# Kernel optimization log

Measured on AMD Instinct MI355X. Metric: run time of the kernel, lower is better.

Reference implementation:

```python
import jax, jax.numpy as jnp
import numpy as np

DIM = 768
NUM_HEADS = 16
HEAD_DIM = DIM // NUM_HEADS  # 48


def setup_inputs() -> dict:
    key = jax.random.key(0)
    ks = jax.random.split(key, 9)
    s = 1.0 / np.sqrt(DIM)
    return {
        "x": jax.random.normal(ks[0], (4, 2048, DIM), dtype=jnp.float32),
        "Wq": jax.random.uniform(ks[1], (DIM, DIM), jnp.float32, -s, s),
        "bq": jax.random.uniform(ks[2], (DIM,), jnp.float32, -s, s),
        "Wk": jax.random.uniform(ks[3], (DIM, DIM), jnp.float32, -s, s),
        "bk": jax.random.uniform(ks[4], (DIM,), jnp.float32, -s, s),
        "Wv": jax.random.uniform(ks[5], (DIM, DIM), jnp.float32, -s, s),
        "bv": jax.random.uniform(ks[6], (DIM,), jnp.float32, -s, s),
        "Wo": jax.random.uniform(ks[7], (DIM, DIM), jnp.float32, -s, s),
        "bo": jax.random.uniform(ks[8], (DIM,), jnp.float32, -s, s),
    }


def reference(x, Wq, bq, Wk, bk, Wv, bv, Wo, bo):
    B, S, D = x.shape
    H, Dh = NUM_HEADS, HEAD_DIM
    # qkv projections -> [B, H, S, Dh]
    q = (x @ Wq.T + bq).reshape(B, S, H, Dh).transpose(0, 2, 1, 3)
    k = (x @ Wk.T + bk).reshape(B, S, H, Dh).transpose(0, 2, 1, 3)
    v = (x @ Wv.T + bv).reshape(B, S, H, Dh).transpose(0, 2, 1, 3)
    scale = 1.0 / np.sqrt(Dh).astype(np.float32)
    scores = jnp.einsum('bhqd,bhkd->bhqk', q, k) * scale  # [B,H,S,S]
    attn = jax.nn.softmax(scores, axis=-1)
    # dropout is identity in eval mode
    out = jnp.einsum('bhqk,bhkd->bhqd', attn, v)  # [B,H,S,Dh]
    out = out.transpose(0, 2, 1, 3).reshape(B, S, D)
    return out @ Wo.T + bo
```

## Files before the change

### kernel.cpp

```cpp
#include <hip/hip_runtime.h>
#include <cstdint>
#include <cstddef>


typedef short s8v __attribute__((ext_vector_type(8)));
typedef float f4v __attribute__((ext_vector_type(4)));
typedef float f16v __attribute__((ext_vector_type(16)));

static constexpr int Bn = 4, Sn = 2048, Dn = 768, Hn = 16, DhN = 48, Dp = 64;
static constexpr int MS = Bn * Sn;

#define MFMA16(a, b, c) __builtin_amdgcn_mfma_f32_16x16x32_bf16((a), (b), (c), 0, 0, 0)
#define MFMA32(a, b, c) __builtin_amdgcn_mfma_f32_32x32x16_bf16((a), (b), (c), 0, 0, 0)

__device__ __forceinline__ int swz4(int r) { return (r + (r >> 2)) & 3; }

__device__ __forceinline__ ushort f2b(float f) {
  return (ushort)((__builtin_bit_cast(uint32_t, f) + 0x8000u) >> 16);
}
__device__ __forceinline__ uint32_t packbf(float a, float b) {
  uint32_t ua = __builtin_bit_cast(uint32_t, a) + 0x8000u;
  uint32_t ub = __builtin_bit_cast(uint32_t, b) + 0x8000u;
  return __builtin_amdgcn_perm(ub, ua, 0x07060302u);
}
__device__ __forceinline__ void pl32swap(uint32_t& a, uint32_t& b) {
  asm("v_permlane32_swap_b32 %0, %1" : "+v"(a), "+v"(b));
}
__device__ __forceinline__ float fexp2(float x) {
  return __builtin_amdgcn_exp2f(x);
}
__device__ __forceinline__ void gload_lds16(const ushort* g, ushort* l) {
  __builtin_amdgcn_global_load_lds(
      (const __attribute__((address_space(1))) uint32_t*)g,
      (__attribute__((address_space(3))) uint32_t*)l, 16, 0, 0);
}

__global__ void cvt_all(const float* __restrict__ x,
                        const float* __restrict__ wq, const float* __restrict__ wk,
                        const float* __restrict__ wv, const float* __restrict__ wo,
                        ushort* __restrict__ xb, ushort* __restrict__ wqkv,
                        ushort* __restrict__ wob) {
  const int bid = blockIdx.x;
  const float* src;
  ushort* dst;
  int i;
  if (bid < 6144) {
    src = x; dst = xb; i = bid * 256 + threadIdx.x;
  } else {
    const int r = (bid - 6144) / 576;
    i = ((bid - 6144) % 576) * 256 + threadIdx.x;
    src = (r == 0) ? wq : (r == 1) ? wk : (r == 2) ? wv : wo;
    dst = (r < 3) ? (wqkv + (size_t)r * Dn * Dn) : wob;
  }
  float4 f = ((const float4*)src)[i];
  ushort4 o = { f2b(f.x), f2b(f.y), f2b(f.z), f2b(f.w) };
  ((ushort4*)dst)[i] = o;
}

__global__ __launch_bounds__(256) void gemm_qkv(
    const ushort* __restrict__ A, const ushort* __restrict__ W,
    const float* __restrict__ bq, const float* __restrict__ bk, const float* __restrict__ bv,
    ushort* __restrict__ outq, ushort* __restrict__ outk, ushort* __restrict__ outv,
    float qscale) {
  __shared__ __align__(16) ushort As[128][64];
  __shared__ __align__(16) ushort Bs[128][64];
  const int tid = threadIdx.x, lane = tid & 63, wave = tid >> 6;
  const int l15 = lane & 15, g = lane >> 4;
  const int m0 = blockIdx.y * 128, n0 = blockIdx.x * 128;
  const int wqm = (wave >> 1) * 64;
  const int wqx = (wave & 1) * 64;
  f4v acc[4][4] = {};

  const ushort* agp[4];
  const ushort* bgp[4];
  ushort* lap[4];
  ushort* lbp[4];
#pragma unroll
  for (int q = 0; q < 4; ++q) {
    const int slot = q * 256 + wave * 64 + lane;
    const int r = slot >> 3, sc = slot & 7;
    const int u = ((((sc & 3) ^ swz4(r & 15)) | (sc & 4)) ^ ((r & 1) << 2)) * 8;
    agp[q] = A + (size_t)(m0 + r) * Dn + u;
    bgp[q] = W + (size_t)(n0 + r) * Dn + u;
    lap[q] = &As[0][0] + slot * 8;
    lbp[q] = &Bs[0][0] + slot * 8;
  }
  const int fcol = (g ^ swz4(l15)) * 8;
  const int par = l15 & 1;

  for (int k0 = 0; k0 < Dn; k0 += 64) {
    __syncthreads();
#pragma unroll
    for (int q = 0; q < 4; ++q) {
      gload_lds16(agp[q] + k0, lap[q]);
      gload_lds16(bgp[q] + k0, lbp[q]);
    }
    __syncthreads();
#pragma unroll
    for (int h = 0; h < 2; ++h) {
      const int fc = fcol + 32 * (h ^ par);
      s8v wf[4], xf[4];
#pragma unroll
      for (int i = 0; i < 4; ++i) wf[i] = *(const s8v*)&Bs[wqm + i * 16 + l15][fc];
#pragma unroll
      for (int j = 0; j < 4; ++j) xf[j] = *(const s8v*)&As[wqx + j * 16 + l15][fc];
#pragma unroll
      for (int i = 0; i < 4; ++i)
#pragma unroll
        for (int j = 0; j < 4; ++j) acc[i][j] = MFMA16(wf[i], xf[j], acc[i][j]);
    }
  }

  const int region = blockIdx.x / 6;
  const int nbase = n0 - region * 768;
  const float* bias = (region == 0) ? bq : (region == 1) ? bk : bv;
#pragma unroll
  for (int i = 0; i < 4; ++i) {
    const int n = nbase + wqm + i * 16 + g * 4;
    const float4 b4 = *(const float4*)&bias[n];
    const int h = n / DhN, dh = n - h * DhN;
#pragma unroll
    for (int j = 0; j < 4; ++j) {
      const int s = m0 + wqx + j * 16 + l15;
      const int b = s >> 11, srow = s & 2047;
      const int bh = b * Hn + h;
      float v0 = acc[i][j][0] + b4.x, v1 = acc[i][j][1] + b4.y;
      float v2 = acc[i][j][2] + b4.z, v3 = acc[i][j][3] + b4.w;
      if (region == 0) { v0 *= qscale; v1 *= qscale; v2 *= qscale; v3 *= qscale; }
      if (region < 2) {
        ushort4 o = { f2b(v0), f2b(v1), f2b(v2), f2b(v3) };
        ushort* dst = region ? outk : outq;
        *(ushort4*)&dst[((size_t)bh * Sn + srow) * Dp + dh] = o;
      } else {
        outv[((size_t)bh * DhN + dh + 0) * Sn + srow] = f2b(v0);
        outv[((size_t)bh * DhN + dh + 1) * Sn + srow] = f2b(v1);
        outv[((size_t)bh * DhN + dh + 2) * Sn + srow] = f2b(v2);
        outv[((size_t)bh * DhN + dh + 3) * Sn + srow] = f2b(v3);
      }
    }
  }
}

__global__ __launch_bounds__(256) void gemm_out(
    const ushort* __restrict__ A, const ushort* __restrict__ W,
    const float* __restrict__ bias, float* __restrict__ out) {
  __shared__ __align__(16) ushort As[128][64];
  __shared__ __align__(16) ushort Bs[128][64];
  const int tid = threadIdx.x, lane = tid & 63, wave = tid >> 6;
  const int l15 = lane & 15, g = lane >> 4;
  const int m0 = blockIdx.y * 128, n0 = blockIdx.x * 128;
  const int wqm = (wave >> 1) * 64;
  const int wqx = (wave & 1) * 64;
  f4v acc[4][4] = {};

  const ushort* agp[4];
  const ushort* bgp[4];
  ushort* lap[4];
  ushort* lbp[4];
#pragma unroll
  for (int q = 0; q < 4; ++q) {
    const int slot = q * 256 + wave * 64 + lane;
    const int r = slot >> 3, sc = slot & 7;
    const int u = ((((sc & 3) ^ swz4(r & 15)) | (sc & 4)) ^ ((r & 1) << 2)) * 8;
    agp[q] = A + (size_t)(m0 + r) * Dn + u;
    bgp[q] = W + (size_t)(n0 + r) * Dn + u;
    lap[q] = &As[0][0] + slot * 8;
    lbp[q] = &Bs[0][0] + slot * 8;
  }
  const int fcol = (g ^ swz4(l15)) * 8;
  const int par = l15 & 1;

  for (int k0 = 0; k0 < Dn; k0 += 64) {
    __syncthreads();
#pragma unroll
    for (int q = 0; q < 4; ++q) {
      gload_lds16(agp[q] + k0, lap[q]);
      gload_lds16(bgp[q] + k0, lbp[q]);
    }
    __syncthreads();
#pragma unroll
    for (int h = 0; h < 2; ++h) {
      const int fc = fcol + 32 * (h ^ par);
      s8v wf[4], xf[4];
#pragma unroll
      for (int i = 0; i < 4; ++i) wf[i] = *(const s8v*)&Bs[wqm + i * 16 + l15][fc];
#pragma unroll
      for (int j = 0; j < 4; ++j) xf[j] = *(const s8v*)&As[wqx + j * 16 + l15][fc];
#pragma unroll
      for (int i = 0; i < 4; ++i)
#pragma unroll
        for (int j = 0; j < 4; ++j) acc[i][j] = MFMA16(wf[i], xf[j], acc[i][j]);
    }
  }

#pragma unroll
  for (int i = 0; i < 4; ++i) {
    const int n = n0 + wqm + i * 16 + g * 4;
    const float4 b4 = *(const float4*)&bias[n];
#pragma unroll
    for (int j = 0; j < 4; ++j) {
      const int s = m0 + wqx + j * 16 + l15;
      float4 o4 = { acc[i][j][0] + b4.x, acc[i][j][1] + b4.y,
                    acc[i][j][2] + b4.z, acc[i][j][3] + b4.w };
      *(float4*)&out[(size_t)s * Dn + n] = o4;
    }
  }
}

__global__ __launch_bounds__(256) void attn_kernel(
    const ushort* __restrict__ qg, const ushort* __restrict__ kg,
    const ushort* __restrict__ vg, ushort* __restrict__ og) {
  __shared__ __align__(16) ushort Ka[128][32];
  __shared__ __align__(16) ushort Kb[128][16];
  __shared__ __align__(16) ushort Vs[64][128];
  const int tid = threadIdx.x;
  const int lane = tid & 63;
  const int wave = tid >> 6;
  const int l31 = lane & 31;
  const int h = lane >> 5;
  const int lin = blockIdx.x + (blockIdx.y << 4);
  const int k8 = lin >> 3;
  const int bh = (lin & 7) * 8 + (k8 >> 4);
  const int q0 = (k8 & 15) * 128;
  const ushort* qb = qg + (size_t)bh * Sn * Dp;
  const ushort* kb = kg + (size_t)bh * Sn * Dp;
  const ushort* vb = vg + (size_t)bh * DhN * Sn;

#pragma unroll
  for (int t = 0; t < 4; ++t) {
    const int idx = tid + t * 256;
    const int row = 48 + (idx >> 6);
    ((uint32_t*)&Vs[row][0])[idx & 63] = (row == 48) ? 0x3F803F80u : 0u;
  }

  s8v qf[3];
#pragma unroll
  for (int kc = 0; kc < 3; ++kc)
    qf[kc] = *(const s8v*)(qb + (size_t)(q0 + wave * 32 + l31) * Dp + kc * 16 + h * 8);

  const ushort* gsrc[6];
  ushort* ldst[6];
  int gstep[6];
#pragma unroll
  for (int t = 0; t < 6; ++t) {
    const int c = wave + 4 * t;
    if (c < 8) {
      const int row = 16 * c + (lane >> 2), j = lane & 3;
      gsrc[t] = kb + (size_t)row * Dp + (j ^ ((row >> 1) & 3)) * 8;
      ldst[t] = &Ka[0][0] + 16 * c * 32 + lane * 8;
      gstep[t] = 128 * Dp;
    } else if (c < 12) {
      const int row = 32 * (c - 8) + (lane >> 1), j = lane & 1;
      gsrc[t] = kb + (size_t)row * Dp + 32 + (j ^ ((row >> 2) & 1)) * 8;
      ldst[t] = &Kb[0][0] + 32 * (c - 8) * 16 + lane * 8;
      gstep[t] = 128 * Dp;
    } else {
      const int row = 4 * (c - 12) + (lane >> 4), j = lane & 15;
      gsrc[t] = vb + (size_t)row * Sn + (j ^ (row & 7)) * 8;
      ldst[t] = &Vs[0][0] + 4 * (c - 12) * 128 + lane * 8;
      gstep[t] = 128;
    }
  }

  f16v o0 = {}, o1 = {};

  for (int kt = 0; kt < Sn; kt += 128) {
    __syncthreads();
#pragma unroll
    for (int t = 0; t < 6; ++t) {
      gload_lds16(gsrc[t], ldst[t]);
      gsrc[t] += gstep[t];
    }
    __syncthreads();

#pragma unroll
    for (int mg = 0; mg < 4; ++mg) {
      const int row = 32 * mg + l31;
      const int s1 = (l31 >> 1) & 3, s2 = (l31 >> 2) & 1;
      s8v a0 = *(const s8v*)&Ka[row][((0 | h) ^ s1) * 8];
      s8v a1 = *(const s8v*)&Ka[row][((2 | h) ^ s1) * 8];
      s8v a2 = *(const s8v*)&Kb[row][((h) ^ s2) * 8];
      f16v sc = {};
      sc = MFMA32(a0, qf[0], sc);
      sc = MFMA32(a1, qf[1], sc);
      sc = MFMA32(a2, qf[2], sc);
      float p[16];
#pragma unroll
      for (int r = 0; r < 16; ++r) p[r] = fexp2(sc[r]);

#pragma unroll
      for (int c2 = 0; c2 < 2; ++c2) {
        const int rb = 8 * c2;
        uint32_t w0 = packbf(p[rb + 0], p[rb + 1]);
        uint32_t w1 = packbf(p[rb + 2], p[rb + 3]);
        uint32_t w2 = packbf(p[rb + 4], p[rb + 5]);
        uint32_t w3 = packbf(p[rb + 6], p[rb + 7]);
        pl32swap(w0, w2);
        pl32swap(w1, w3);
        uint4 af = { w0, w1, w2, w3 };
        const s8v pa = __builtin_bit_cast(s8v, af);
        const int kcv = 2 * mg + c2;
        const int vc = ((2 * kcv + h) ^ (l31 & 7)) * 8;
        const s8v v0 = *(const s8v*)&Vs[l31][vc];
        const s8v v1 = *(const s8v*)&Vs[32 + l31][vc];
        o0 = MFMA32(pa, v0, o0);
        o1 = MFMA32(pa, v1, o1);
      }
    }
  }

  const int b = bh >> 4, hh = bh & 15;
#pragma unroll
  for (int r = 0; r < 16; ++r) {
    const int q = (r & 3) + 8 * (r >> 2) + 4 * h;
    const float lsum = __shfl(o1[r], 16 + (lane & 32), 64);
    const float inv = 1.0f / lsum;
    const int s = q0 + wave * 32 + q;
    const size_t base = ((size_t)(b * Sn + s)) * Dn + hh * DhN;
    og[base + l31] = f2b(o0[r] * inv);
    if (l31 < 16) og[base + 32 + l31] = f2b(o1[r] * inv);
  }
}

extern "C" void kernel_launch(void* const* d_in, const int* in_sizes, int n_in,
                              void* d_out, int out_size, void* d_ws, size_t ws_size,
                              hipStream_t stream) {
  (void)in_sizes; (void)n_in; (void)out_size; (void)ws_size;
  const float* x  = (const float*)d_in[0];
  const float* Wq = (const float*)d_in[1];
  const float* bq = (const float*)d_in[2];
  const float* Wk = (const float*)d_in[3];
  const float* bk = (const float*)d_in[4];
  const float* Wv = (const float*)d_in[5];
  const float* bv = (const float*)d_in[6];
  const float* Wo = (const float*)d_in[7];
  const float* bo = (const float*)d_in[8];

  size_t off = 0;
  auto alloc = [&](size_t bytes) {
    void* p = (char*)d_ws + off;
    off += (bytes + 255) & ~(size_t)255;
    return p;
  };
  ushort* xb    = (ushort*)alloc((size_t)MS * Dn * 2);
  ushort* Wqkvb = (ushort*)alloc((size_t)3 * Dn * Dn * 2);
  ushort* Wob   = (ushort*)alloc((size_t)Dn * Dn * 2);
  ushort* qbuf  = (ushort*)alloc((size_t)Bn * Hn * Sn * Dp * 2);
  ushort* kbuf  = (ushort*)alloc((size_t)Bn * Hn * Sn * Dp * 2);
  ushort* vbuf  = (ushort*)alloc((size_t)Bn * Hn * DhN * Sn * 2);
  ushort* ao    = (ushort*)alloc((size_t)MS * Dn * 2);

  cvt_all<<<6144 + 4 * 576, 256, 0, stream>>>(x, Wq, Wk, Wv, Wo, xb, Wqkvb, Wob);

  const dim3 blk(256);
  const float qscale = 0.20823510929813633f;
  gemm_qkv<<<dim3(18, MS / 128), blk, 0, stream>>>(xb, Wqkvb, bq, bk, bv,
                                                   qbuf, kbuf, vbuf, qscale);

  attn_kernel<<<dim3(Sn / 128, Bn * Hn), blk, 0, stream>>>(qbuf, kbuf, vbuf, ao);

  gemm_out<<<dim3(6, MS / 128), blk, 0, stream>>>(ao, Wob, bo, (float*)d_out);
}
```

Measured before the change: 245.0 us.

## Split attention over key halves with a separate combine kernel

Adds a split-K attention path. Each of two grid slices processes half of the keys and writes unnormalized fp32 partial outputs, with the row sum carried in an extra ones-row of V, to a workspace buffer. A combine kernel then adds the two halves, normalizes and writes bf16. This doubles the number of attention blocks to improve occupancy and load balance across CUs, at the cost of extra global traffic for the partials and one more launch. It relies on there being no running max, so the exp values must stay in range. The path runs only when the workspace is large enough, otherwise it falls back to the original kernel.

```diff
diff --git a/kernel.cpp b/kernel.cpp
--- a/kernel.cpp
+++ b/kernel.cpp
@@ -204,6 +204,142 @@
                     acc[i][j][2] + b4.z, acc[i][j][3] + b4.w };
       *(float4*)&out[(size_t)s * Dn + n] = o4;
     }
+  }
+}
+
+__global__ __launch_bounds__(256) void attn_split(
+    const ushort* __restrict__ qg, const ushort* __restrict__ kg,
+    const ushort* __restrict__ vg, float* __restrict__ pbuf) {
+  __shared__ __align__(16) ushort Ka[64][32];
+  __shared__ __align__(16) ushort Kb[64][16];
+  __shared__ __align__(16) ushort Vs[64][64];
+  const int tid = threadIdx.x;
+  const int lane = tid & 63;
+  const int wave = tid >> 6;
+  const int l31 = lane & 31;
+  const int h = lane >> 5;
+  const int kh = blockIdx.z;
+  const int lin = blockIdx.x + (blockIdx.y << 4);
+  const int k8 = lin >> 3;
+  const int bh = (lin & 7) * 8 + (k8 >> 4);
+  const int q0 = (k8 & 15) * 128;
+  const ushort* qb = qg + (size_t)bh * Sn * Dp;
+  const ushort* kb = kg + (size_t)bh * Sn * Dp + (size_t)kh * 1024 * Dp;
+  const ushort* vb = vg + (size_t)bh * DhN * Sn + kh * 1024;
+
+#pragma unroll
+  for (int t = 0; t < 2; ++t) {
+    const int idx = tid + t * 256;
+    const int row = 48 + (idx >> 5);
+    ((uint32_t*)&Vs[row][0])[idx & 31] = (row == 48) ? 0x3F803F80u : 0u;
+  }
+
+  s8v qf[3];
+#pragma unroll
+  for (int kc = 0; kc < 3; ++kc)
+    qf[kc] = *(const s8v*)(qb + (size_t)(q0 + wave * 32 + l31) * Dp + kc * 16 + h * 8);
+
+  const ushort* gsrc[3];
+  ushort* ldst[3];
+  int gstep[3];
+#pragma unroll
+  for (int t = 0; t < 3; ++t) {
+    const int c = wave + 4 * t;
+    if (c < 4) {
+      const int row = 16 * c + (lane >> 2), j = lane & 3;
+      gsrc[t] = kb + (size_t)row * Dp + (j ^ ((row >> 1) & 3)) * 8;
+      ldst[t] = &Ka[0][0] + 16 * c * 32 + lane * 8;
+      gstep[t] = 64 * Dp;
+    } else if (c < 6) {
+      const int row = 32 * (c - 4) + (lane >> 1), j = lane & 1;
+      gsrc[t] = kb + (size_t)row * Dp + 32 + (j ^ ((row >> 2) & 1)) * 8;
+      ldst[t] = &Kb[0][0] + 32 * (c - 4) * 16 + lane * 8;
+      gstep[t] = 64 * Dp;
+    } else {
+      const int row = 8 * (c - 6) + (lane >> 3), j = lane & 7;
+      gsrc[t] = vb + (size_t)row * Sn + (j ^ (row & 7)) * 8;
+      ldst[t] = &Vs[0][0] + 8 * (c - 6) * 64 + lane * 8;
+      gstep[t] = 64;
+    }
+  }
+
+  f16v o0 = {}, o1 = {};
+
+  for (int kt = 0; kt < 1024; kt += 64) {
+    __syncthreads();
+#pragma unroll
+    for (int t = 0; t < 3; ++t) {
+      gload_lds16(gsrc[t], ldst[t]);
+      gsrc[t] += gstep[t];
+    }
+    __syncthreads();
+
+#pragma unroll
+    for (int mg = 0; mg < 2; ++mg) {
+      const int row = 32 * mg + l31;
+      const int s1 = (l31 >> 1) & 3, s2 = (l31 >> 2) & 1;
+      s8v a0 = *(const s8v*)&Ka[row][((0 | h) ^ s1) * 8];
+      s8v a1 = *(const s8v*)&Ka[row][((2 | h) ^ s1) * 8];
+      s8v a2 = *(const s8v*)&Kb[row][((h) ^ s2) * 8];
+      f16v sc = {};
+      sc = MFMA32(a0, qf[0], sc);
+      sc = MFMA32(a1, qf[1], sc);
+      sc = MFMA32(a2, qf[2], sc);
+      float p[16];
+#pragma unroll
+      for (int r = 0; r < 16; ++r) p[r] = fexp2(sc[r]);
+
+#pragma unroll
+      for (int c2 = 0; c2 < 2; ++c2) {
+        const int rb = 8 * c2;
+        uint32_t w0 = packbf(p[rb + 0], p[rb + 1]);
+        uint32_t w1 = packbf(p[rb + 2], p[rb + 3]);
+        uint32_t w2 = packbf(p[rb + 4], p[rb + 5]);
+        uint32_t w3 = packbf(p[rb + 6], p[rb + 7]);
+        pl32swap(w0, w2);
+        pl32swap(w1, w3);
+        uint4 af = { w0, w1, w2, w3 };
+        const s8v pa = __builtin_bit_cast(s8v, af);
+        const int kcv = 2 * mg + c2;
+        const int vc = ((2 * kcv + h) ^ (l31 & 7)) * 8;
+        const s8v v0 = *(const s8v*)&Vs[l31][vc];
+        const s8v v1 = *(const s8v*)&Vs[32 + l31][vc];
+        o0 = MFMA32(pa, v0, o0);
+        o1 = MFMA32(pa, v1, o1);
+      }
+    }
+  }
+
+  const int qt = q0 >> 7;
+  float* pb = pbuf + ((size_t)kh * 1024 + bh * 16 + qt) * 8192;
+#pragma unroll
+  for (int r = 0; r < 16; ++r) {
+    const int q = (r & 3) + 8 * (r >> 2) + 4 * h;
+    const int sl = wave * 32 + q;
+    pb[sl * 64 + l31] = o0[r];
+    pb[sl * 64 + 32 + l31] = o1[r];
+  }
+}
+
+__global__ __launch_bounds__(256) void attn_combine(
+    const float* __restrict__ pb, ushort* __restrict__ og) {
+  const int bid = blockIdx.x;
+  const int bh = bid >> 4, qt = bid & 15;
+  const int b = bh >> 4, hh = bh & 15;
+  const float* p0 = pb + (size_t)bid * 8192;
+  const float* p1 = p0 + (size_t)1024 * 8192;
+  const int tid = threadIdx.x;
+#pragma unroll
+  for (int it = 0; it < 6; ++it) {
+    const int i4 = tid + 256 * it;
+    const int q = i4 / 12, c4 = i4 - q * 12;
+    const float l = p0[q * 64 + 48] + p1[q * 64 + 48];
+    const float inv = 1.0f / l;
+    const float4 a = *(const float4*)&p0[q * 64 + c4 * 4];
+    const float4 c = *(const float4*)&p1[q * 64 + c4 * 4];
+    ushort4 o = { f2b((a.x + c.x) * inv), f2b((a.y + c.y) * inv),
+                  f2b((a.z + c.z) * inv), f2b((a.w + c.w) * inv) };
+    *(ushort4*)&og[((size_t)(b * Sn + qt * 128 + q)) * Dn + hh * DhN + c4 * 4] = o;
   }
 }
 
@@ -325,7 +461,7 @@
 extern "C" void kernel_launch(void* const* d_in, const int* in_sizes, int n_in,
                               void* d_out, int out_size, void* d_ws, size_t ws_size,
                               hipStream_t stream) {
-  (void)in_sizes; (void)n_in; (void)out_size; (void)ws_size;
+  (void)in_sizes; (void)n_in; (void)out_size;
   const float* x  = (const float*)d_in[0];
   const float* Wq = (const float*)d_in[1];
   const float* bq = (const float*)d_in[2];
@@ -349,6 +485,8 @@
   ushort* kbuf  = (ushort*)alloc((size_t)Bn * Hn * Sn * Dp * 2);
   ushort* vbuf  = (ushort*)alloc((size_t)Bn * Hn * DhN * Sn * 2);
   ushort* ao    = (ushort*)alloc((size_t)MS * Dn * 2);
+  float*  pbuf  = (float*)alloc((size_t)2 * 1024 * 128 * 64 * 4);
+  const bool split = (off <= ws_size);
 
   cvt_all<<<6144 + 4 * 576, 256, 0, stream>>>(x, Wq, Wk, Wv, Wo, xb, Wqkvb, Wob);
 
@@ -357,7 +495,12 @@
   gemm_qkv<<<dim3(18, MS / 128), blk, 0, stream>>>(xb, Wqkvb, bq, bk, bv,
                                                    qbuf, kbuf, vbuf, qscale);
 
-  attn_kernel<<<dim3(Sn / 128, Bn * Hn), blk, 0, stream>>>(qbuf, kbuf, vbuf, ao);
+  if (split) {
+    attn_split<<<dim3(Sn / 128, Bn * Hn, 2), blk, 0, stream>>>(qbuf, kbuf, vbuf, pbuf);
+    attn_combine<<<dim3(Bn * Hn * 16), blk, 0, stream>>>(pbuf, ao);
+  } else {
+    attn_kernel<<<dim3(Sn / 128, Bn * Hn), blk, 0, stream>>>(qbuf, kbuf, vbuf, ao);
+  }
 
   gemm_out<<<dim3(6, MS / 128), blk, 0, stream>>>(ao, Wob, bo, (float*)d_out);
 }
```

New measurement: 255.6 us. 1.04x slower.

## Split attention KV range across two wave groups per block and reduce via LDS

Applied to the files above, without the earlier changes.

The attention kernel now launches 512 threads per block. Two groups of four waves each process half of the key/value sequence, with smaller 64-key tiles staged in separate LDS halves. The partial unnormalized outputs and row sums are combined through LDS scratch before normalization and store. This doubles the waves available per query tile to hide latency, at the cost of extra barriers, an LDS reduction, and more synchronization per iteration.

```diff
diff --git a/kernel.cpp b/kernel.cpp
--- a/kernel.cpp
+++ b/kernel.cpp
@@ -207,15 +207,15 @@
   }
 }
 
-__global__ __launch_bounds__(256) void attn_kernel(
-    const ushort* __restrict__ qg, const ushort* __restrict__ kg,
+__global__ __launch_bounds__(512) void attn_fused(
+    const ushort* __restrict__ qg, const ushort* __restrict__ kgl,
     const ushort* __restrict__ vg, ushort* __restrict__ og) {
-  __shared__ __align__(16) ushort Ka[128][32];
-  __shared__ __align__(16) ushort Kb[128][16];
-  __shared__ __align__(16) ushort Vs[64][128];
+  __shared__ __align__(16) ushort smem[2][7168];
   const int tid = threadIdx.x;
   const int lane = tid & 63;
   const int wave = tid >> 6;
+  const int w4 = wave & 3;
+  const int kg = wave >> 2;
   const int l31 = lane & 31;
   const int h = lane >> 5;
   const int lin = blockIdx.x + (blockIdx.y << 4);
@@ -223,63 +223,62 @@
   const int bh = (lin & 7) * 8 + (k8 >> 4);
   const int q0 = (k8 & 15) * 128;
   const ushort* qb = qg + (size_t)bh * Sn * Dp;
-  const ushort* kb = kg + (size_t)bh * Sn * Dp;
-  const ushort* vb = vg + (size_t)bh * DhN * Sn;
-
-#pragma unroll
-  for (int t = 0; t < 4; ++t) {
-    const int idx = tid + t * 256;
-    const int row = 48 + (idx >> 6);
-    ((uint32_t*)&Vs[row][0])[idx & 63] = (row == 48) ? 0x3F803F80u : 0u;
-  }
+  const ushort* kb = kgl + (size_t)bh * Sn * Dp + (size_t)kg * 1024 * Dp;
+  const ushort* vb = vg + (size_t)bh * DhN * Sn + kg * 1024;
+  ushort* KaH = &smem[kg][0];
+  ushort* KbH = &smem[kg][2048];
+  ushort* VsH = &smem[kg][3072];
+
+  ((uint32_t*)&smem[0][6144])[tid] = (tid < 32) ? 0x3F803F80u : 0u;
+  ((uint32_t*)&smem[1][6144])[tid] = (tid < 32) ? 0x3F803F80u : 0u;
 
   s8v qf[3];
 #pragma unroll
   for (int kc = 0; kc < 3; ++kc)
-    qf[kc] = *(const s8v*)(qb + (size_t)(q0 + wave * 32 + l31) * Dp + kc * 16 + h * 8);
-
-  const ushort* gsrc[6];
-  ushort* ldst[6];
-  int gstep[6];
-#pragma unroll
-  for (int t = 0; t < 6; ++t) {
-    const int c = wave + 4 * t;
-    if (c < 8) {
+    qf[kc] = *(const s8v*)(qb + (size_t)(q0 + w4 * 32 + l31) * Dp + kc * 16 + h * 8);
+
+  const ushort* gsrc[3];
+  ushort* ldst[3];
+  int gstep[3];
+#pragma unroll
+  for (int t = 0; t < 3; ++t) {
+    const int c = w4 + 4 * t;
+    if (c < 4) {
       const int row = 16 * c + (lane >> 2), j = lane & 3;
       gsrc[t] = kb + (size_t)row * Dp + (j ^ ((row >> 1) & 3)) * 8;
-      ldst[t] = &Ka[0][0] + 16 * c * 32 + lane * 8;
-      gstep[t] = 128 * Dp;
-    } else if (c < 12) {
-      const int row = 32 * (c - 8) + (lane >> 1), j = lane & 1;
+      ldst[t] = KaH + 16 * c * 32 + lane * 8;
+      gstep[t] = 64 * Dp;
+    } else if (c < 6) {
+      const int row = 32 * (c - 4) + (lane >> 1), j = lane & 1;
       gsrc[t] = kb + (size_t)row * Dp + 32 + (j ^ ((row >> 2) & 1)) * 8;
-      ldst[t] = &Kb[0][0] + 32 * (c - 8) * 16 + lane * 8;
-      gstep[t] = 128 * Dp;
+      ldst[t] = KbH + 32 * (c - 4) * 16 + lane * 8;
+      gstep[t] = 64 * Dp;
     } else {
-      const int row = 4 * (c - 12) + (lane >> 4), j = lane & 15;
+      const int row = 8 * (c - 6) + (lane >> 3), j = lane & 7;
       gsrc[t] = vb + (size_t)row * Sn + (j ^ (row & 7)) * 8;
-      ldst[t] = &Vs[0][0] + 4 * (c - 12) * 128 + lane * 8;
-      gstep[t] = 128;
+      ldst[t] = VsH + 8 * (c - 6) * 64 + lane * 8;
+      gstep[t] = 64;
     }
   }
 
   f16v o0 = {}, o1 = {};
 
-  for (int kt = 0; kt < Sn; kt += 128) {
-    __syncthreads();
-#pragma unroll
-    for (int t = 0; t < 6; ++t) {
+  for (int kt = 0; kt < 1024; kt += 64) {
+    __syncthreads();
+#pragma unroll
+    for (int t = 0; t < 3; ++t) {
       gload_lds16(gsrc[t], ldst[t]);
       gsrc[t] += gstep[t];
     }
     __syncthreads();
 
 #pragma unroll
-    for (int mg = 0; mg < 4; ++mg) {
+    for (int mg = 0; mg < 2; ++mg) {
       const int row = 32 * mg + l31;
       const int s1 = (l31 >> 1) & 3, s2 = (l31 >> 2) & 1;
-      s8v a0 = *(const s8v*)&Ka[row][((0 | h) ^ s1) * 8];
-      s8v a1 = *(const s8v*)&Ka[row][((2 | h) ^ s1) * 8];
-      s8v a2 = *(const s8v*)&Kb[row][((h) ^ s2) * 8];
+      s8v a0 = *(const s8v*)(KaH + row * 32 + ((0 | h) ^ s1) * 8);
+      s8v a1 = *(const s8v*)(KaH + row * 32 + ((2 | h) ^ s1) * 8);
+      s8v a2 = *(const s8v*)(KbH + row * 16 + ((h) ^ s2) * 8);
       f16v sc = {};
       sc = MFMA32(a0, qf[0], sc);
       sc = MFMA32(a1, qf[1], sc);
@@ -301,24 +300,46 @@
         const s8v pa = __builtin_bit_cast(s8v, af);
         const int kcv = 2 * mg + c2;
         const int vc = ((2 * kcv + h) ^ (l31 & 7)) * 8;
-        const s8v v0 = *(const s8v*)&Vs[l31][vc];
-        const s8v v1 = *(const s8v*)&Vs[32 + l31][vc];
+        const s8v v0 = *(const s8v*)(VsH + l31 * 64 + vc);
+        const s8v v1 = *(const s8v*)(VsH + (32 + l31) * 64 + vc);
         o0 = MFMA32(pa, v0, o0);
         o1 = MFMA32(pa, v1, o1);
       }
     }
   }
 
-  const int b = bh >> 4, hh = bh & 15;
-#pragma unroll
-  for (int r = 0; r < 16; ++r) {
-    const int q = (r & 3) + 8 * (r >> 2) + 4 * h;
-    const float lsum = __shfl(o1[r], 16 + (lane & 32), 64);
-    const float inv = 1.0f / lsum;
-    const int s = q0 + wave * 32 + q;
-    const size_t base = ((size_t)(b * Sn + s)) * Dn + hh * DhN;
-    og[base + l31] = f2b(o0[r] * inv);
-    if (l31 < 16) og[base + 32 + l31] = f2b(o1[r] * inv);
+  __syncthreads();
+  float* scr = (float*)&smem[0][0];
+  if (kg == 1) {
+#pragma unroll
+    for (int r = 0; r < 16; ++r) scr[r * 256 + w4 * 64 + lane] = o0[r];
+  }
+  __syncthreads();
+  if (kg == 0) {
+#pragma unroll
+    for (int r = 0; r < 16; ++r) o0[r] += scr[r * 256 + w4 * 64 + lane];
+  }
+  __syncthreads();
+  if (kg == 1) {
+#pragma unroll
+    for (int r = 0; r < 16; ++r) scr[r * 256 + w4 * 64 + lane] = o1[r];
+  }
+  __syncthreads();
+  if (kg == 0) {
+#pragma unroll
+    for (int r = 0; r < 16; ++r) o1[r] += scr[r * 256 + w4 * 64 + lane];
+
+    const int b = bh >> 4, hh = bh & 15;
+#pragma unroll
+    for (int r = 0; r < 16; ++r) {
+      const int q = (r & 3) + 8 * (r >> 2) + 4 * h;
+      const float lsum = __shfl(o1[r], 16 + (lane & 32), 64);
+      const float inv = 1.0f / lsum;
+      const int s = q0 + w4 * 32 + q;
+      const size_t base = ((size_t)(b * Sn + s)) * Dn + hh * DhN;
+      og[base + l31] = f2b(o0[r] * inv);
+      if (l31 < 16) og[base + 32 + l31] = f2b(o1[r] * inv);
+    }
   }
 }
 
@@ -357,7 +378,7 @@
   gemm_qkv<<<dim3(18, MS / 128), blk, 0, stream>>>(xb, Wqkvb, bq, bk, bv,
                                                    qbuf, kbuf, vbuf, qscale);
 
-  attn_kernel<<<dim3(Sn / 128, Bn * Hn), blk, 0, stream>>>(qbuf, kbuf, vbuf, ao);
+  attn_fused<<<dim3(Sn / 128, Bn * Hn), dim3(512), 0, stream>>>(qbuf, kbuf, vbuf, ao);
 
   gemm_out<<<dim3(6, MS / 128), blk, 0, stream>>>(ao, Wob, bo, (float*)d_out);
 }
```

Result: faster. 237.8 us (-3.0%).
